# Performance work log

Measured on AMD Instinct MI355X. Metric: run time of the kernel, lower is better.

Reference implementation:

```python
import jax, jax.numpy as jnp
import numpy as np


def setup_inputs() -> dict:
    key = jax.random.key(0)
    # [batch, time, num_classes] logits, as fed to the Keras layer
    logits = jax.random.normal(key, (256, 1024, 128), dtype=jnp.float32)
    return {"logits": logits}


def reference(logits):
    """CTC greedy decode (merge_repeated=True) + sparse_to_dense with default -1.

    TF's ctc_greedy_decoder uses blank = num_classes - 1. The TF layer's dense
    output width is the max decoded length over the batch (data-dependent);
    here we pad to the static maximum T, extra columns are filled with -1,
    which matches the TF result up to trailing all -1 padding columns.
    """
    B, T, C = logits.shape
    blank = C - 1

    am = jnp.argmax(logits, axis=-1)                       # [B, T] best class per step
    prev = jnp.concatenate(
        [jnp.full((B, 1), -1, dtype=am.dtype), am[:, :-1]], axis=1
    )                                                      # previous step's argmax
    keep = (am != prev) & (am != blank)                    # collapse repeats, drop blanks

    pos = jnp.cumsum(keep.astype(jnp.int32), axis=1) - 1   # compacted column per kept token
    col = jnp.where(keep, pos, T)                          # dropped tokens scatter to a dump column

    rows = jnp.broadcast_to(jnp.arange(B)[:, None], (B, T))
    out = jnp.full((B, T + 1), -1, dtype=jnp.int32)
    out = out.at[rows, col].set(jnp.where(keep, am, -1).astype(jnp.int32))
    return out[:, :T]                                      # drop dump column -> [B, T]
```

## Files before the change

kernel.cpp:

```cpp
#include <hip/hip_runtime.h>


constexpr int B = 256;
constexpr int T = 1024;
constexpr int C = 128;
constexpr int BLANK = C - 1;

__global__ __launch_bounds__(256)
void ctc_argmax_kernel(const float* __restrict__ logits, int* __restrict__ am) {
    const int tid  = threadIdx.x;
    const int lane = tid & 63;
    const int wid  = tid >> 6;
    const int row  = blockIdx.x >> 4;
    const int chunk = blockIdx.x & 15;

    const int t     = chunk * 64 + wid * 16 + (lane >> 2);
    const int csub  = (lane & 3) * 4;

    const float* p = logits + ((size_t)row * T + t) * C + csub;

    float4 v[8];
    #pragma unroll
    for (int i = 0; i < 8; ++i)
        v[i] = *reinterpret_cast<const float4*>(p + 16 * i);

    float best = v[0].x; int bidx = csub;
    #pragma unroll
    for (int i = 0; i < 8; ++i) {
        const int cb = csub + 16 * i;
        if (i > 0 && v[i].x > best) { best = v[i].x; bidx = cb; }
        if (v[i].y > best) { best = v[i].y; bidx = cb + 1; }
        if (v[i].z > best) { best = v[i].z; bidx = cb + 2; }
        if (v[i].w > best) { best = v[i].w; bidx = cb + 3; }
    }

    #pragma unroll
    for (int off = 1; off <= 2; off <<= 1) {
        float ov = __shfl_xor(best, off, 64);
        int   oi = __shfl_xor(bidx, off, 64);
        if (ov > best || (ov == best && oi < bidx)) { best = ov; bidx = oi; }
    }

    if ((lane & 3) == 0) am[(size_t)row * T + t] = bidx;
}

__global__ __launch_bounds__(1024)
void ctc_scan_kernel(const int* __restrict__ am, int* __restrict__ out) {
    const int b    = blockIdx.x;
    const int tid  = threadIdx.x;
    const int lane = tid & 63;
    const int wid  = tid >> 6;

    __shared__ int wsum[16];

    const int* arow = am + (size_t)b * T;
    const int a    = arow[tid];
    const int prev = (tid > 0) ? arow[tid - 1] : -1;
    const int keep = (a != prev && a != BLANK) ? 1 : 0;

    int scan = keep;
    #pragma unroll
    for (int off = 1; off <= 32; off <<= 1) {
        int n = __shfl_up(scan, off, 64);
        if (lane >= off) scan += n;
    }
    if (lane == 63) wsum[wid] = scan;
    __syncthreads();

    int waveOff = 0, total = 0;
    #pragma unroll
    for (int w = 0; w < 16; ++w) {
        const int s = wsum[w];
        if (w < wid) waveOff += s;
        total += s;
    }

    int* orow = out + (size_t)b * T;
    if (keep) orow[waveOff + scan - 1] = a;
    if (tid >= total) orow[tid] = -1;
}

extern "C" void kernel_launch(void* const* d_in, const int* in_sizes, int n_in,
                              void* d_out, int out_size, void* d_ws, size_t ws_size,
                              hipStream_t stream) {
    const float* logits = (const float*)d_in[0];
    int* out = (int*)d_out;
    int* am  = (int*)d_ws;

    ctc_argmax_kernel<<<B * (T / 64), 256, 0, stream>>>(logits, am);
    ctc_scan_kernel<<<B, 1024, 0, stream>>>(am, out);
}
```

Baseline: 27.42 us.

## Fuse argmax and scan into one per-row kernel with shared-memory argmax

Merges the argmax and compaction kernels into a single kernel with one 1024-thread block per batch row. The block keeps the per-step argmax in shared memory instead of a global workspace. This removes a kernel launch and the global write and read of the intermediate argmax array. In exchange, the grid shrinks to one block per row, which lowers memory-level parallelism and raises register pressure from the unrolled loads.

```diff
diff --git a/kernel.cpp b/kernel.cpp
--- a/kernel.cpp
+++ b/kernel.cpp
@@ -6,56 +6,53 @@
 constexpr int C = 128;
 constexpr int BLANK = C - 1;
 
-__global__ __launch_bounds__(256)
-void ctc_argmax_kernel(const float* __restrict__ logits, int* __restrict__ am) {
-    const int tid  = threadIdx.x;
-    const int lane = tid & 63;
-    const int wid  = tid >> 6;
-    const int row  = blockIdx.x >> 4;
-    const int chunk = blockIdx.x & 15;
-
-    const int t     = chunk * 64 + wid * 16 + (lane >> 2);
-    const int csub  = (lane & 3) * 4;
-
-    const float* p = logits + ((size_t)row * T + t) * C + csub;
-
-    float4 v[8];
-    #pragma unroll
-    for (int i = 0; i < 8; ++i)
-        v[i] = *reinterpret_cast<const float4*>(p + 16 * i);
-
-    float best = v[0].x; int bidx = csub;
-    #pragma unroll
-    for (int i = 0; i < 8; ++i) {
-        const int cb = csub + 16 * i;
-        if (i > 0 && v[i].x > best) { best = v[i].x; bidx = cb; }
-        if (v[i].y > best) { best = v[i].y; bidx = cb + 1; }
-        if (v[i].z > best) { best = v[i].z; bidx = cb + 2; }
-        if (v[i].w > best) { best = v[i].w; bidx = cb + 3; }
-    }
-
-    #pragma unroll
-    for (int off = 1; off <= 2; off <<= 1) {
-        float ov = __shfl_xor(best, off, 64);
-        int   oi = __shfl_xor(bidx, off, 64);
-        if (ov > best || (ov == best && oi < bidx)) { best = ov; bidx = oi; }
-    }
-
-    if ((lane & 3) == 0) am[(size_t)row * T + t] = bidx;
-}
-
-__global__ __launch_bounds__(1024)
-void ctc_scan_kernel(const int* __restrict__ am, int* __restrict__ out) {
+__global__ __launch_bounds__(1024, 4)
+void ctc_fused_kernel(const float* __restrict__ logits, int* __restrict__ out) {
     const int b    = blockIdx.x;
     const int tid  = threadIdx.x;
     const int lane = tid & 63;
     const int wid  = tid >> 6;
 
+    __shared__ int am[T];
     __shared__ int wsum[16];
 
-    const int* arow = am + (size_t)b * T;
-    const int a    = arow[tid];
-    const int prev = (tid > 0) ? arow[tid - 1] : -1;
+    const float* row = logits + (size_t)b * T * C;
+
+    const int csub = (tid & 3) * 4;
+
+    #pragma unroll
+    for (int k = 0; k < 4; ++k) {
+        const int t = k * 256 + (tid >> 2);
+        const float* p = row + (size_t)t * C + csub;
+
+        float4 v[8];
+        #pragma unroll
+        for (int i = 0; i < 8; ++i)
+            v[i] = *reinterpret_cast<const float4*>(p + 16 * i);
+
+        float best = v[0].x; int bidx = csub;
+        #pragma unroll
+        for (int i = 0; i < 8; ++i) {
+            const int cb = csub + 16 * i;
+            if (i > 0 && v[i].x > best) { best = v[i].x; bidx = cb; }
+            if (v[i].y > best) { best = v[i].y; bidx = cb + 1; }
+            if (v[i].z > best) { best = v[i].z; bidx = cb + 2; }
+            if (v[i].w > best) { best = v[i].w; bidx = cb + 3; }
+        }
+
+        #pragma unroll
+        for (int off = 1; off <= 2; off <<= 1) {
+            float ov = __shfl_xor(best, off, 64);
+            int   oi = __shfl_xor(bidx, off, 64);
+            if (ov > best || (ov == best && oi < bidx)) { best = ov; bidx = oi; }
+        }
+
+        if ((tid & 3) == 0) am[t] = bidx;
+    }
+    __syncthreads();
+
+    const int a    = am[tid];
+    const int prev = (tid > 0) ? am[tid - 1] : -1;
     const int keep = (a != prev && a != BLANK) ? 1 : 0;
 
     int scan = keep;
@@ -85,8 +82,5 @@
                               hipStream_t stream) {
     const float* logits = (const float*)d_in[0];
     int* out = (int*)d_out;
-    int* am  = (int*)d_ws;
-
-    ctc_argmax_kernel<<<B * (T / 64), 256, 0, stream>>>(logits, am);
-    ctc_scan_kernel<<<B, 1024, 0, stream>>>(am, out);
+    ctc_fused_kernel<<<B, 1024, 0, stream>>>(logits, out);
 }
```

New measurement: 26.57 us. 3.1% less time.
